# Optimization experiments

Hardware: AMD Instinct MI355X
Metric: run time of the kernel (lower is better)

## Reference

```python
import math
import jax, jax.numpy as jnp
import numpy as np

# ---- SLAYER neuron / simulation constants (from config) ----
THETA = 10.0      # spike threshold
TAU_SR = 10.0     # PSP (SRM) kernel time constant
TAU_REF = 1.0     # refractory kernel time constant
TS = 1.0          # simulation time step
T_SAMPLE = 500    # number of time bins
B, N_IN, N_HID, N_OUT = 64, 1024, 1024, 10


def _alpha_kernel(tau, mult, eps=0.01):
    """slayer _calculateAlphaKernel: mult * t/tau * exp(1 - t/tau), truncated."""
    vals = []
    t = 0.0
    while t < T_SAMPLE:
        v = mult * t / tau * math.exp(1.0 - t / tau)
        if abs(v) < eps and t > tau:
            break
        vals.append(v)
        t += TS
    return np.asarray(vals, np.float32)

SRM_KERNEL = jnp.asarray(_alpha_kernel(TAU_SR, 1.0))            # [K]
REF_KERNEL = jnp.asarray(_alpha_kernel(TAU_REF, -2.0 * THETA))  # [Kr], REF_KERNEL[0] == 0


def dense(x, W):
    # per-timestep fully-connected layer (slayer.dense == 1x1x1 conv3d, no bias)
    # x: [B, Nin, T], W: [Nout, Nin] -> [B, Nout, T]
    return jnp.einsum('oi,bit->bot', W, x)


def psp(x):
    # causal temporal convolution with the SRM kernel: out[t] = Ts * sum_k srm[k] * x[t-k]
    Bx, N, T = x.shape
    K = SRM_KERNEL.shape[0]
    k = SRM_KERNEL[::-1].reshape(1, 1, K).astype(x.dtype)  # flip -> true convolution
    y = jax.lax.conv_general_dilated(
        x.reshape(Bx * N, 1, T), k, (1,), [(K - 1, 0)],
        dimension_numbers=('NCH', 'OIH', 'NCH'))
    return y.reshape(Bx, N, T) * TS


def spike_impl(u_in):
    # sequential LIF thresholding with refractory feedback (slayer spike kernel)
    # u_in: [B, N, T] membrane drive; returns (spikes, membrane) both [B, N, T]
    Kr = REF_KERNEL.shape[0]
    # buf[j] is the refractory contribution arriving at step t+j; new spike at t
    # contributes REF_KERNEL[j] at t+j (REF_KERNEL[0]==0), i.e. shifted kernel into buf.
    refk = jnp.concatenate([REF_KERNEL[1:], jnp.zeros((1,), u_in.dtype)]).astype(u_in.dtype)
    buf0 = jnp.zeros(u_in.shape[:-1] + (Kr,), u_in.dtype)

    def step(buf, u_t):
        u = u_t + buf[..., 0]                              # membrane at time t
        s = (u >= THETA).astype(u_in.dtype) / TS           # spike (amplitude 1/Ts)
        buf = jnp.concatenate([buf[..., 1:], jnp.zeros_like(buf[..., :1])], axis=-1)
        buf = buf + s[..., None] * refk
        return buf, (s, u)

    _, (s, u) = jax.lax.scan(step, buf0, jnp.moveaxis(u_in, -1, 0))
    return jnp.moveaxis(s, 0, -1), jnp.moveaxis(u, 0, -1)


def setup_inputs() -> dict:
    key = jax.random.key(0)
    k1, k2, k3 = jax.random.split(key, 3)
    spike_input = (jax.random.uniform(k1, (B, N_IN, T_SAMPLE)) < 0.05).astype(jnp.float32)
    W1 = jax.random.normal(k2, (N_HID, N_IN), jnp.float32) * 0.3
    W2 = jax.random.normal(k3, (N_OUT, N_HID), jnp.float32) * 0.3
    return {"spike_input": spike_input, "W1": W1, "W2": W2}


def reference(spike_input, W1, W2):
    s1, _ = spike_impl(psp(dense(spike_input, W1)))
    s2, _ = spike_impl(psp(dense(s1, W2)))
    return s2
```

## Files before the change

kernel.cpp:

```cpp
#include <hip/hip_runtime.h>
#include <stdint.h>
#include <math.h>

#define T_SIM 500
#define NB    64
#define NIN   1024
#define NHID  1024
#define NOUT  10
#define KSRM  77
#define CHUNK 32
#define TT5   12
#define NT5   42
#define RINGN 104

__device__ __forceinline__ double srm_tap(int k) {
  double u = (double)k / 10.0;
  double v = u * exp(1.0 - u);
  return (double)(float)v;
}
__device__ __forceinline__ double ref_tap(int j) {
  double v = (-20.0 * (double)j) * exp(1.0 - (double)j);
  return (double)(float)v;
}

__global__ __launch_bounds__(64)
void k_pack(const float* __restrict__ x, unsigned long long* __restrict__ bits) {
  const int b = blockIdx.x, ig = blockIdx.y, tc = blockIdx.z;
  const int lane = threadIdx.x;
  const float* xr = x + ((size_t)b * NIN + ig * 64 + lane) * T_SIM;
  const int t0 = tc * 100;
  for (int t = t0; t < t0 + 100; t += 4) {
    const float4 v = *(const float4*)(xr + t);
    unsigned long long m0 = __ballot(v.x > 0.5f);
    unsigned long long m1 = __ballot(v.y > 0.5f);
    unsigned long long m2 = __ballot(v.z > 0.5f);
    unsigned long long m3 = __ballot(v.w > 0.5f);
    if (lane == 0) {
      unsigned long long* w = bits + (size_t)(b * T_SIM + t) * 16 + ig;
      w[0] = m0; w[16] = m1; w[32] = m2; w[48] = m3;
    }
  }
}

__global__ __launch_bounds__(256)
void k_transpose(const float* __restrict__ W1, float* __restrict__ W1T) {
  __shared__ float tile[64][65];
  const int bo = blockIdx.x * 64, bi = blockIdx.y * 64;
  for (int k = threadIdx.x; k < 4096; k += 256) {
    int r = k >> 6, c = k & 63;
    tile[r][c] = W1[(size_t)(bo + r) * NIN + bi + c];
  }
  __syncthreads();
  for (int k = threadIdx.x; k < 4096; k += 256) {
    int r = k >> 6, c = k & 63;
    W1T[(size_t)(bi + r) * NHID + bo + c] = tile[c][r];
  }
}

__global__ __launch_bounds__(128)
void k_dense1(const uint32_t* __restrict__ bits, const float* __restrict__ W1T,
              double* __restrict__ a1c, int col_base) {
  __shared__ int list[NIN];
  __shared__ int nact_s;
  const int col_loc = blockIdx.x;
  const int tid = threadIdx.x;
  if (tid < 32) {
    uint32_t w = bits[(size_t)(col_base + col_loc) * 32 + tid];
    int c = __popc(w);
    int p = c;
#pragma unroll
    for (int d = 1; d < 32; d <<= 1) {
      int q = __shfl_up(p, d);
      if (tid >= d) p += q;
    }
    int excl = p - c;
    while (w) {
      const int j = __ffs(w) - 1;
      w &= w - 1;
      list[excl++] = tid * 32 + j;
    }
    if (tid == 31) nact_s = excl;
  }
  __syncthreads();
  const int n = nact_s;
  const int o = blockIdx.y * 512 + tid * 4;
  double ax[4] = {0,0,0,0}, ay[4] = {0,0,0,0};
  double az[4] = {0,0,0,0}, aw[4] = {0,0,0,0};
  float4 L[8];
  int g = 0;
  if (n >= 8) {
#pragma unroll
    for (int r = 0; r < 8; ++r)
      L[r] = *(const float4*)(W1T + (size_t)list[r] * NHID + o);
    for (g = 0; g + 16 <= n; g += 8) {
      float4 Nb[8];
#pragma unroll
      for (int r = 0; r < 8; ++r)
        Nb[r] = *(const float4*)(W1T + (size_t)list[g + 8 + r] * NHID + o);
#pragma unroll
      for (int r = 0; r < 8; ++r) {
        const int s = r & 3;
        ax[s] += (double)L[r].x; ay[s] += (double)L[r].y;
        az[s] += (double)L[r].z; aw[s] += (double)L[r].w;
      }
#pragma unroll
      for (int r = 0; r < 8; ++r) L[r] = Nb[r];
    }
#pragma unroll
    for (int r = 0; r < 8; ++r) {
      const int s = r & 3;
      ax[s] += (double)L[r].x; ay[s] += (double)L[r].y;
      az[s] += (double)L[r].z; aw[s] += (double)L[r].w;
    }
    g += 8;
  }
  for (; g < n; ++g) {
    const float4 wv = *(const float4*)(W1T + (size_t)list[g] * NHID + o);
    const int s = g & 3;
    ax[s] += (double)wv.x; ay[s] += (double)wv.y;
    az[s] += (double)wv.z; aw[s] += (double)wv.w;
  }
  double* dst = a1c + (size_t)col_loc * NHID + o;
  __builtin_nontemporal_store((ax[0] + ax[1]) + (ax[2] + ax[3]), dst + 0);
  __builtin_nontemporal_store((ay[0] + ay[1]) + (ay[2] + ay[3]), dst + 1);
  __builtin_nontemporal_store((az[0] + az[1]) + (az[2] + az[3]), dst + 2);
  __builtin_nontemporal_store((aw[0] + aw[1]) + (aw[2] + aw[3]), dst + 3);
}

__global__ __launch_bounds__(448)
void k_ps1(const double* __restrict__ a1c, uint32_t* __restrict__ s1w,
           int b_base) {
  __shared__ double S[RINGN * 32];
  __shared__ double Yp[2][4][TT5 * 32];
  __shared__ double TB[80];
  const int ng = blockIdx.x, b_loc = blockIdx.y;
  const int tid = threadIdx.x;
  const double* __restrict__ abase = a1c + (size_t)b_loc * T_SIM * NHID + ng * 32;
  uint32_t* __restrict__ sbase = s1w + (size_t)(b_base + b_loc) * T_SIM * 32 + ng;

  if (tid < 80) TB[tid] = (tid <= 76) ? srm_tap(tid) : 0.0;
  for (int i = tid; i < RINGN * 32; i += 448) S[i] = 0.0;
  __syncthreads();
  for (int id = tid; id < TT5 * 32; id += 448) {
    const int r = id >> 5, nn = id & 31;
    S[r * 32 + nn] = abase[(size_t)r * NHID + nn];
  }

  const bool isFIR = (tid < 384);
  const int g   = tid / 96;
  const int rem = tid - g * 96;
  const int q   = rem >> 5;
  const int n   = rem & 31;
  double tap[20];
  __syncthreads();
  if (isFIR) {
#pragma unroll
    for (int j = 0; j < 20; ++j) tap[j] = TB[20 * g + j];
  }
  double refk[11];
#pragma unroll
  for (int j = 1; j <= 10; ++j) refk[j] = ref_tap(j);
  uint32_t smask = 0;

  for (int k = 0; k < NT5; ++k) {
    const int t0 = k * TT5;
    const int tv = (T_SIM - t0 < TT5) ? (T_SIM - t0) : TT5;
    const int t0n = t0 + TT5;
    const int tvn = (t0n >= T_SIM) ? 0 : ((T_SIM - t0n < TT5) ? (T_SIM - t0n) : TT5);
    if (isFIR) {
      double pf = 0.0;
      const int pr = tid >> 5, pn = tid & 31;
      const bool hasPf = (tid < tvn * 32);
      if (hasPf) pf = abase[(size_t)(t0n + pr) * NHID + pn];
      const int tb = t0 + q * 4;
      int slot = (tb - 20 * g - 19 + 10400) % RINGN;
      double a0 = 0, a1 = 0, a2 = 0, a3 = 0;
#pragma unroll
      for (int s = 0; s < 23; ++s) {
        const double v = S[slot * 32 + n];
        slot = slot + 1;
        if (slot == RINGN) slot = 0;
        if (s <= 19)           a0 += tap[19 - s] * v;
        if (s >= 1 && s <= 20) a1 += tap[20 - s] * v;
        if (s >= 2 && s <= 21) a2 += tap[21 - s] * v;
        if (s >= 3)            a3 += tap[22 - s] * v;
      }
      double* Yk = Yp[k & 1][g];
      const int tl = q * 4;
      if (tl + 0 < tv) Yk[(tl + 0) * 32 + n] = a0;
      if (tl + 1 < tv) Yk[(tl + 1) * 32 + n] = a1;
      if (tl + 2 < tv) Yk[(tl + 2) * 32 + n] = a2;
      if (tl + 3 < tv) Yk[(tl + 3) * 32 + n] = a3;
      if (hasPf) S[((t0n + pr) % RINGN) * 32 + pn] = pf;
    } else if (k > 0) {
      const int lane = tid - 384;
      if (lane < 32) {
        const int t0p = t0 - TT5;
        const double* Y0 = Yp[(k - 1) & 1][0];
        const double* Y1 = Yp[(k - 1) & 1][1];
        const double* Y2 = Yp[(k - 1) & 1][2];
        const double* Y3 = Yp[(k - 1) & 1][3];
        for (int gg = 0; gg < TT5; ++gg) {
          double u = (Y0[gg * 32 + lane] + Y1[gg * 32 + lane]) +
                     (Y2[gg * 32 + lane] + Y3[gg * 32 + lane]);
#pragma unroll
          for (int j = 10; j >= 1; --j)
            u += refk[j] * (double)((smask >> (j - 1)) & 1u);
          const bool sp = (u >= 10.0);
          smask = (smask << 1) | (sp ? 1u : 0u);
          const unsigned long long bm = __ballot(sp);
          if (lane == 0) sbase[(size_t)(t0p + gg) * 32] = (uint32_t)bm;
        }
      }
    }
    __syncthreads();
  }
  if (!isFIR) {
    const int lane = tid - 384;
    if (lane < 32) {
      const int t0p = (NT5 - 1) * TT5;
      const int tvp = T_SIM - t0p;
      const double* Y0 = Yp[(NT5 - 1) & 1][0];
      const double* Y1 = Yp[(NT5 - 1) & 1][1];
      const double* Y2 = Yp[(NT5 - 1) & 1][2];
      const double* Y3 = Yp[(NT5 - 1) & 1][3];
      for (int gg = 0; gg < tvp; ++gg) {
        double u = (Y0[gg * 32 + lane] + Y1[gg * 32 + lane]) +
                   (Y2[gg * 32 + lane] + Y3[gg * 32 + lane]);
#pragma unroll
        for (int j = 10; j >= 1; --j)
          u += refk[j] * (double)((smask >> (j - 1)) & 1u);
        const bool sp = (u >= 10.0);
        smask = (smask << 1) | (sp ? 1u : 0u);
        const unsigned long long bm = __ballot(sp);
        if (lane == 0) sbase[(size_t)(t0p + gg) * 32] = (uint32_t)bm;
      }
    }
  }
}

__global__ __launch_bounds__(256)
void k_dense2(const uint32_t* __restrict__ s1w,
              const float* __restrict__ W2, double* __restrict__ a2) {
  __shared__ float w2t[NHID * NOUT];
  for (int k = threadIdx.x; k < NHID * NOUT; k += 256) {
    const int o = k >> 10, i = k & 1023;
    w2t[i * NOUT + o] = W2[k];
  }
  __syncthreads();
  const int col = blockIdx.x * 256 + threadIdx.x;
  double acc[NOUT];
#pragma unroll
  for (int o = 0; o < NOUT; ++o) acc[o] = 0.0;
  const uint32_t* w = s1w + (size_t)col * 32;
  for (int wi = 0; wi < 32; ++wi) {
    uint32_t m = w[wi];
    const int ibase = wi * 32;
    while (m) {
      const int j = __ffs(m) - 1;
      m &= m - 1;
      const float* row = &w2t[(ibase + j) * NOUT];
#pragma unroll
      for (int o = 0; o < NOUT; ++o) acc[o] += (double)row[o];
    }
  }
  double* outp = a2 + (size_t)col * NOUT;
#pragma unroll
  for (int o = 0; o < NOUT; ++o) outp[o] = acc[o];
}

__global__ __launch_bounds__(256)
void k_l2(const double* __restrict__ a2, float* __restrict__ out) {
  __shared__ double S[T_SIM * NOUT];
  __shared__ double Y[T_SIM * NOUT];
  __shared__ double srm[KSRM];
  const int b = blockIdx.x, tid = threadIdx.x;
  if (tid < KSRM) srm[tid] = srm_tap(tid);
  for (int i = tid; i < T_SIM * NOUT; i += 256)
    S[i] = a2[(size_t)b * T_SIM * NOUT + i];
  __syncthreads();
  for (int i = tid; i < T_SIM * NOUT; i += 256) {
    const int t = i / 10, o = i - t * 10;
    const int kmax = (t < KSRM - 1) ? t : (KSRM - 1);
    double acc = 0.0;
    for (int k = 0; k <= kmax; ++k)
      acc += srm[k] * S[(t - k) * 10 + o];
    Y[i] = acc;
  }
  __syncthreads();
  if (tid < NOUT) {
    double refk[11];
#pragma unroll
    for (int j = 1; j <= 10; ++j) refk[j] = ref_tap(j);
    uint32_t smask = 0;
    float* op = out + ((size_t)b * NOUT + tid) * T_SIM;
    for (int t = 0; t < T_SIM; ++t) {
      double u = Y[t * 10 + tid];
#pragma unroll
      for (int j = 10; j >= 1; --j)
        u += refk[j] * (double)((smask >> (j - 1)) & 1u);
      const bool sp = (u >= 10.0);
      smask = (smask << 1) | (sp ? 1u : 0u);
      op[t] = sp ? 1.0f : 0.0f;
    }
  }
}

extern "C" void kernel_launch(void* const* d_in, const int* in_sizes, int n_in,
                              void* d_out, int out_size, void* d_ws, size_t ws_size,
                              hipStream_t stream) {
  const float* x  = (const float*)d_in[0];
  const float* W1 = (const float*)d_in[1];
  const float* W2 = (const float*)d_in[2];
  float* out = (float*)d_out;

  char* ws = (char*)d_ws;
  unsigned long long* bits1 = (unsigned long long*)(ws);
  float*  W1T = (float*) (ws + 4096000);
  double* a1c = (double*)(ws + 8290304);
  uint32_t* s1w = (uint32_t*)(ws + 139362304);
  double* a2  = (double*)(ws + 143458304);

  hipLaunchKernelGGL(k_pack, dim3(NB, 16, 5), dim3(64), 0, stream, x, bits1);
  hipLaunchKernelGGL(k_transpose, dim3(16, 16), dim3(256), 0, stream, W1, W1T);

  for (int bc = 0; bc < NB; bc += CHUNK) {
    hipLaunchKernelGGL(k_dense1, dim3(CHUNK * T_SIM, 2), dim3(128), 0, stream,
                       (const uint32_t*)bits1, W1T, a1c, bc * T_SIM);
    hipLaunchKernelGGL(k_ps1, dim3(32, CHUNK), dim3(448), 0, stream,
                       a1c, s1w, bc);
  }

  hipLaunchKernelGGL(k_dense2, dim3(125), dim3(256), 0, stream, s1w, W2, a2);
  hipLaunchKernelGGL(k_l2, dim3(NB), dim3(256), 0, stream, a2, out);
}
```

Before: 956.9 us.

## Fuse dense1 and PSP/spike stages into one kernel pipelined across double-buffered chunks

Merges the dense1 and PSP/spike kernels into a single kernel whose blocks are split by block index into dense-column work and PSP work. Chunk c's dense accumulation runs concurrently with chunk c-1's PSP/spike pass, using two ping-pong activation buffers. The batch chunk is halved to 16 and the dense part now uses 256 of the 448 threads with one block per column, so the PSP stage's serial latency is meant to hide under dense throughput. In exchange, 192 threads sit idle in every dense block, and the shared-memory union and 448-thread launch bounds may lower occupancy.

```diff
diff --git a/kernel.cpp b/kernel.cpp
--- a/kernel.cpp
+++ b/kernel.cpp
@@ -8,10 +8,11 @@
 #define NHID  1024
 #define NOUT  10
 #define KSRM  77
-#define CHUNK 32
+#define CHUNK 16
 #define TT5   12
 #define NT5   42
 #define RINGN 104
+#define NGW   32
 
 __device__ __forceinline__ double srm_tap(int k) {
   double u = (double)k / 10.0;
@@ -57,152 +58,122 @@
   }
 }
 
-__global__ __launch_bounds__(128)
-void k_dense1(const uint32_t* __restrict__ bits, const float* __restrict__ W1T,
-              double* __restrict__ a1c, int col_base) {
-  __shared__ int list[NIN];
-  __shared__ int nact_s;
-  const int col_loc = blockIdx.x;
+__global__ __launch_bounds__(448, 4)
+void k_fused(const uint32_t* __restrict__ bits, const float* __restrict__ W1T,
+             double* __restrict__ aw, const double* __restrict__ ar,
+             uint32_t* __restrict__ s1w, int col_base, int ndense, int nps1,
+             int b_base) {
+  __shared__ union U {
+    struct { double S[RINGN * NGW]; double Yp[2][4][TT5 * NGW]; double TB[80]; } p;
+    struct { int list[NIN]; int nact; } d;
+  } sh;
+  const int bid = blockIdx.x;
   const int tid = threadIdx.x;
-  if (tid < 32) {
-    uint32_t w = bits[(size_t)(col_base + col_loc) * 32 + tid];
-    int c = __popc(w);
-    int p = c;
-#pragma unroll
-    for (int d = 1; d < 32; d <<= 1) {
-      int q = __shfl_up(p, d);
-      if (tid >= d) p += q;
-    }
-    int excl = p - c;
-    while (w) {
-      const int j = __ffs(w) - 1;
-      w &= w - 1;
-      list[excl++] = tid * 32 + j;
-    }
-    if (tid == 31) nact_s = excl;
-  }
-  __syncthreads();
-  const int n = nact_s;
-  const int o = blockIdx.y * 512 + tid * 4;
-  double ax[4] = {0,0,0,0}, ay[4] = {0,0,0,0};
-  double az[4] = {0,0,0,0}, aw[4] = {0,0,0,0};
-  float4 L[8];
-  int g = 0;
-  if (n >= 8) {
-#pragma unroll
-    for (int r = 0; r < 8; ++r)
-      L[r] = *(const float4*)(W1T + (size_t)list[r] * NHID + o);
-    for (g = 0; g + 16 <= n; g += 8) {
-      float4 Nb[8];
-#pragma unroll
-      for (int r = 0; r < 8; ++r)
-        Nb[r] = *(const float4*)(W1T + (size_t)list[g + 8 + r] * NHID + o);
-#pragma unroll
-      for (int r = 0; r < 8; ++r) {
-        const int s = r & 3;
-        ax[s] += (double)L[r].x; ay[s] += (double)L[r].y;
-        az[s] += (double)L[r].z; aw[s] += (double)L[r].w;
+  int dcol = -1, pblk = -1;
+  if (ndense && nps1) {
+    const int q = bid / 17, r = bid - 17 * q;
+    if (r == 16) pblk = q; else dcol = q * 16 + r;
+  } else if (nps1) {
+    pblk = bid;
+  } else {
+    dcol = bid;
+  }
+
+  if (pblk >= 0) {
+    if (pblk >= nps1) return;
+    const int ng = pblk & 31, b_loc = pblk >> 5;
+    const double* __restrict__ abase = ar + (size_t)b_loc * T_SIM * NHID + ng * NGW;
+    uint32_t* __restrict__ sbase = s1w + (size_t)(b_base + b_loc) * T_SIM * 32 + ng;
+
+    if (tid < 80) sh.p.TB[tid] = (tid <= 76) ? srm_tap(tid) : 0.0;
+    for (int i = tid; i < RINGN * NGW; i += 448) sh.p.S[i] = 0.0;
+    __syncthreads();
+    for (int id = tid; id < TT5 * NGW; id += 448) {
+      const int r = id >> 5, nn = id & 31;
+      sh.p.S[r * NGW + nn] = abase[(size_t)r * NHID + nn];
+    }
+
+    const bool isFIR = (tid < 384);
+    const int g   = tid / 96;
+    const int rem = tid - g * 96;
+    const int q   = rem >> 5;
+    const int n   = rem & 31;
+    double tap[20];
+    __syncthreads();
+    if (isFIR) {
+#pragma unroll
+      for (int j = 0; j < 20; ++j) tap[j] = sh.p.TB[20 * g + j];
+    }
+    double refk[11];
+#pragma unroll
+    for (int j = 1; j <= 10; ++j) refk[j] = ref_tap(j);
+    uint32_t smask = 0;
+
+    for (int k = 0; k < NT5; ++k) {
+      const int t0 = k * TT5;
+      const int tv = (T_SIM - t0 < TT5) ? (T_SIM - t0) : TT5;
+      const int t0n = t0 + TT5;
+      const int tvn = (t0n >= T_SIM) ? 0 : ((T_SIM - t0n < TT5) ? (T_SIM - t0n) : TT5);
+      if (isFIR) {
+        double pf = 0.0;
+        const int pr = tid >> 5, pn = tid & 31;
+        const bool hasPf = (tid < tvn * NGW);
+        if (hasPf) pf = abase[(size_t)(t0n + pr) * NHID + pn];
+        const int tb = t0 + q * 4;
+        int slot = (tb - 20 * g - 19 + 10400) % RINGN;
+        double a0 = 0, a1 = 0, a2 = 0, a3 = 0;
+#pragma unroll
+        for (int s = 0; s < 23; ++s) {
+          const double v = sh.p.S[slot * NGW + n];
+          slot = slot + 1;
+          if (slot == RINGN) slot = 0;
+          if (s <= 19)           a0 += tap[19 - s] * v;
+          if (s >= 1 && s <= 20) a1 += tap[20 - s] * v;
+          if (s >= 2 && s <= 21) a2 += tap[21 - s] * v;
+          if (s >= 3)            a3 += tap[22 - s] * v;
+        }
+        double* Yk = sh.p.Yp[k & 1][g];
+        const int tl = q * 4;
+        if (tl + 0 < tv) Yk[(tl + 0) * NGW + n] = a0;
+        if (tl + 1 < tv) Yk[(tl + 1) * NGW + n] = a1;
+        if (tl + 2 < tv) Yk[(tl + 2) * NGW + n] = a2;
+        if (tl + 3 < tv) Yk[(tl + 3) * NGW + n] = a3;
+        if (hasPf) sh.p.S[((t0n + pr) % RINGN) * NGW + pn] = pf;
+      } else if (k > 0) {
+        const int lane = tid - 384;
+        if (lane < 32) {
+          const int t0p = t0 - TT5;
+          const double* Y0 = sh.p.Yp[(k - 1) & 1][0];
+          const double* Y1 = sh.p.Yp[(k - 1) & 1][1];
+          const double* Y2 = sh.p.Yp[(k - 1) & 1][2];
+          const double* Y3 = sh.p.Yp[(k - 1) & 1][3];
+          for (int gg = 0; gg < TT5; ++gg) {
+            double u = (Y0[gg * NGW + lane] + Y1[gg * NGW + lane]) +
+                       (Y2[gg * NGW + lane] + Y3[gg * NGW + lane]);
+#pragma unroll
+            for (int j = 10; j >= 1; --j)
+              u += refk[j] * (double)((smask >> (j - 1)) & 1u);
+            const bool sp = (u >= 10.0);
+            smask = (smask << 1) | (sp ? 1u : 0u);
+            const unsigned long long bm = __ballot(sp);
+            if (lane == 0) sbase[(size_t)(t0p + gg) * 32] = (uint32_t)bm;
+          }
+        }
       }
-#pragma unroll
-      for (int r = 0; r < 8; ++r) L[r] = Nb[r];
-    }
-#pragma unroll
-    for (int r = 0; r < 8; ++r) {
-      const int s = r & 3;
-      ax[s] += (double)L[r].x; ay[s] += (double)L[r].y;
-      az[s] += (double)L[r].z; aw[s] += (double)L[r].w;
-    }
-    g += 8;
-  }
-  for (; g < n; ++g) {
-    const float4 wv = *(const float4*)(W1T + (size_t)list[g] * NHID + o);
-    const int s = g & 3;
-    ax[s] += (double)wv.x; ay[s] += (double)wv.y;
-    az[s] += (double)wv.z; aw[s] += (double)wv.w;
-  }
-  double* dst = a1c + (size_t)col_loc * NHID + o;
-  __builtin_nontemporal_store((ax[0] + ax[1]) + (ax[2] + ax[3]), dst + 0);
-  __builtin_nontemporal_store((ay[0] + ay[1]) + (ay[2] + ay[3]), dst + 1);
-  __builtin_nontemporal_store((az[0] + az[1]) + (az[2] + az[3]), dst + 2);
-  __builtin_nontemporal_store((aw[0] + aw[1]) + (aw[2] + aw[3]), dst + 3);
-}
-
-__global__ __launch_bounds__(448)
-void k_ps1(const double* __restrict__ a1c, uint32_t* __restrict__ s1w,
-           int b_base) {
-  __shared__ double S[RINGN * 32];
-  __shared__ double Yp[2][4][TT5 * 32];
-  __shared__ double TB[80];
-  const int ng = blockIdx.x, b_loc = blockIdx.y;
-  const int tid = threadIdx.x;
-  const double* __restrict__ abase = a1c + (size_t)b_loc * T_SIM * NHID + ng * 32;
-  uint32_t* __restrict__ sbase = s1w + (size_t)(b_base + b_loc) * T_SIM * 32 + ng;
-
-  if (tid < 80) TB[tid] = (tid <= 76) ? srm_tap(tid) : 0.0;
-  for (int i = tid; i < RINGN * 32; i += 448) S[i] = 0.0;
-  __syncthreads();
-  for (int id = tid; id < TT5 * 32; id += 448) {
-    const int r = id >> 5, nn = id & 31;
-    S[r * 32 + nn] = abase[(size_t)r * NHID + nn];
-  }
-
-  const bool isFIR = (tid < 384);
-  const int g   = tid / 96;
-  const int rem = tid - g * 96;
-  const int q   = rem >> 5;
-  const int n   = rem & 31;
-  double tap[20];
-  __syncthreads();
-  if (isFIR) {
-#pragma unroll
-    for (int j = 0; j < 20; ++j) tap[j] = TB[20 * g + j];
-  }
-  double refk[11];
-#pragma unroll
-  for (int j = 1; j <= 10; ++j) refk[j] = ref_tap(j);
-  uint32_t smask = 0;
-
-  for (int k = 0; k < NT5; ++k) {
-    const int t0 = k * TT5;
-    const int tv = (T_SIM - t0 < TT5) ? (T_SIM - t0) : TT5;
-    const int t0n = t0 + TT5;
-    const int tvn = (t0n >= T_SIM) ? 0 : ((T_SIM - t0n < TT5) ? (T_SIM - t0n) : TT5);
-    if (isFIR) {
-      double pf = 0.0;
-      const int pr = tid >> 5, pn = tid & 31;
-      const bool hasPf = (tid < tvn * 32);
-      if (hasPf) pf = abase[(size_t)(t0n + pr) * NHID + pn];
-      const int tb = t0 + q * 4;
-      int slot = (tb - 20 * g - 19 + 10400) % RINGN;
-      double a0 = 0, a1 = 0, a2 = 0, a3 = 0;
-#pragma unroll
-      for (int s = 0; s < 23; ++s) {
-        const double v = S[slot * 32 + n];
-        slot = slot + 1;
-        if (slot == RINGN) slot = 0;
-        if (s <= 19)           a0 += tap[19 - s] * v;
-        if (s >= 1 && s <= 20) a1 += tap[20 - s] * v;
-        if (s >= 2 && s <= 21) a2 += tap[21 - s] * v;
-        if (s >= 3)            a3 += tap[22 - s] * v;
-      }
-      double* Yk = Yp[k & 1][g];
-      const int tl = q * 4;
-      if (tl + 0 < tv) Yk[(tl + 0) * 32 + n] = a0;
-      if (tl + 1 < tv) Yk[(tl + 1) * 32 + n] = a1;
-      if (tl + 2 < tv) Yk[(tl + 2) * 32 + n] = a2;
-      if (tl + 3 < tv) Yk[(tl + 3) * 32 + n] = a3;
-      if (hasPf) S[((t0n + pr) % RINGN) * 32 + pn] = pf;
-    } else if (k > 0) {
+      __syncthreads();
+    }
+    if (!isFIR) {
       const int lane = tid - 384;
       if (lane < 32) {
-        const int t0p = t0 - TT5;
-        const double* Y0 = Yp[(k - 1) & 1][0];
-        const double* Y1 = Yp[(k - 1) & 1][1];
-        const double* Y2 = Yp[(k - 1) & 1][2];
-        const double* Y3 = Yp[(k - 1) & 1][3];
-        for (int gg = 0; gg < TT5; ++gg) {
-          double u = (Y0[gg * 32 + lane] + Y1[gg * 32 + lane]) +
-                     (Y2[gg * 32 + lane] + Y3[gg * 32 + lane]);
+        const int t0p = (NT5 - 1) * TT5;
+        const int tvp = T_SIM - t0p;
+        const double* Y0 = sh.p.Yp[(NT5 - 1) & 1][0];
+        const double* Y1 = sh.p.Yp[(NT5 - 1) & 1][1];
+        const double* Y2 = sh.p.Yp[(NT5 - 1) & 1][2];
+        const double* Y3 = sh.p.Yp[(NT5 - 1) & 1][3];
+        for (int gg = 0; gg < tvp; ++gg) {
+          double u = (Y0[gg * NGW + lane] + Y1[gg * NGW + lane]) +
+                     (Y2[gg * NGW + lane] + Y3[gg * NGW + lane]);
 #pragma unroll
           for (int j = 10; j >= 1; --j)
             u += refk[j] * (double)((smask >> (j - 1)) & 1u);
@@ -213,29 +184,73 @@
         }
       }
     }
-    __syncthreads();
-  }
-  if (!isFIR) {
-    const int lane = tid - 384;
-    if (lane < 32) {
-      const int t0p = (NT5 - 1) * TT5;
-      const int tvp = T_SIM - t0p;
-      const double* Y0 = Yp[(NT5 - 1) & 1][0];
-      const double* Y1 = Yp[(NT5 - 1) & 1][1];
-      const double* Y2 = Yp[(NT5 - 1) & 1][2];
-      const double* Y3 = Yp[(NT5 - 1) & 1][3];
-      for (int gg = 0; gg < tvp; ++gg) {
-        double u = (Y0[gg * 32 + lane] + Y1[gg * 32 + lane]) +
-                   (Y2[gg * 32 + lane] + Y3[gg * 32 + lane]);
-#pragma unroll
-        for (int j = 10; j >= 1; --j)
-          u += refk[j] * (double)((smask >> (j - 1)) & 1u);
-        const bool sp = (u >= 10.0);
-        smask = (smask << 1) | (sp ? 1u : 0u);
-        const unsigned long long bm = __ballot(sp);
-        if (lane == 0) sbase[(size_t)(t0p + gg) * 32] = (uint32_t)bm;
+    return;
+  }
+
+  if (dcol >= ndense) return;
+  const int col_loc = dcol;
+  if (tid < 32) {
+    uint32_t w = bits[(size_t)(col_base + col_loc) * 32 + tid];
+    int c = __popc(w);
+    int p = c;
+#pragma unroll
+    for (int d = 1; d < 32; d <<= 1) {
+      int qq = __shfl_up(p, d);
+      if (tid >= d) p += qq;
+    }
+    int excl = p - c;
+    while (w) {
+      const int j = __ffs(w) - 1;
+      w &= w - 1;
+      sh.d.list[excl++] = tid * 32 + j;
+    }
+    if (tid == 31) sh.d.nact = excl;
+  }
+  __syncthreads();
+  if (tid < 256) {
+    const int n = sh.d.nact;
+    const int o = tid * 4;
+    double ax[4] = {0,0,0,0}, ay[4] = {0,0,0,0};
+    double az[4] = {0,0,0,0}, aw4[4] = {0,0,0,0};
+    float4 L[8];
+    int g = 0;
+    if (n >= 8) {
+#pragma unroll
+      for (int r = 0; r < 8; ++r)
+        L[r] = *(const float4*)(W1T + (size_t)sh.d.list[r] * NHID + o);
+      for (g = 0; g + 16 <= n; g += 8) {
+        float4 Nb[8];
+#pragma unroll
+        for (int r = 0; r < 8; ++r)
+          Nb[r] = *(const float4*)(W1T + (size_t)sh.d.list[g + 8 + r] * NHID + o);
+#pragma unroll
+        for (int r = 0; r < 8; ++r) {
+          const int s = r & 3;
+          ax[s] += (double)L[r].x; ay[s] += (double)L[r].y;
+          az[s] += (double)L[r].z; aw4[s] += (double)L[r].w;
+        }
+#pragma unroll
+        for (int r = 0; r < 8; ++r) L[r] = Nb[r];
       }
-    }
+#pragma unroll
+      for (int r = 0; r < 8; ++r) {
+        const int s = r & 3;
+        ax[s] += (double)L[r].x; ay[s] += (double)L[r].y;
+        az[s] += (double)L[r].z; aw4[s] += (double)L[r].w;
+      }
+      g += 8;
+    }
+    for (; g < n; ++g) {
+      const float4 wv = *(const float4*)(W1T + (size_t)sh.d.list[g] * NHID + o);
+      const int s = g & 3;
+      ax[s] += (double)wv.x; ay[s] += (double)wv.y;
+      az[s] += (double)wv.z; aw4[s] += (double)wv.w;
+    }
+    double* dst = aw + (size_t)col_loc * NHID + o;
+    __builtin_nontemporal_store((ax[0] + ax[1]) + (ax[2] + ax[3]), dst + 0);
+    __builtin_nontemporal_store((ay[0] + ay[1]) + (ay[2] + ay[3]), dst + 1);
+    __builtin_nontemporal_store((az[0] + az[1]) + (az[2] + az[3]), dst + 2);
+    __builtin_nontemporal_store((aw4[0] + aw4[1]) + (aw4[2] + aw4[3]), dst + 3);
   }
 }
 
@@ -316,20 +331,29 @@
 
   char* ws = (char*)d_ws;
   unsigned long long* bits1 = (unsigned long long*)(ws);
-  float*  W1T = (float*) (ws + 4096000);
-  double* a1c = (double*)(ws + 8290304);
+  float*  W1T = (float*)(ws + 4096000);
+  double* abuf0 = (double*)(ws + 8290304);
+  double* abuf1 = (double*)(ws + 73826304);
   uint32_t* s1w = (uint32_t*)(ws + 139362304);
   double* a2  = (double*)(ws + 143458304);
+  double* abuf[2] = {abuf0, abuf1};
 
   hipLaunchKernelGGL(k_pack, dim3(NB, 16, 5), dim3(64), 0, stream, x, bits1);
   hipLaunchKernelGGL(k_transpose, dim3(16, 16), dim3(256), 0, stream, W1, W1T);
 
-  for (int bc = 0; bc < NB; bc += CHUNK) {
-    hipLaunchKernelGGL(k_dense1, dim3(CHUNK * T_SIM, 2), dim3(128), 0, stream,
-                       (const uint32_t*)bits1, W1T, a1c, bc * T_SIM);
-    hipLaunchKernelGGL(k_ps1, dim3(32, CHUNK), dim3(448), 0, stream,
-                       a1c, s1w, bc);
-  }
+  const int NDB = CHUNK * T_SIM;
+  const int NPB = 32 * CHUNK;
+  hipLaunchKernelGGL(k_fused, dim3(NDB), dim3(448), 0, stream,
+                     (const uint32_t*)bits1, W1T, abuf[0], abuf[1], s1w,
+                     0, NDB, 0, 0);
+  for (int c = 1; c < 4; ++c) {
+    hipLaunchKernelGGL(k_fused, dim3(17 * NPB), dim3(448), 0, stream,
+                       (const uint32_t*)bits1, W1T, abuf[c & 1], abuf[(c ^ 1) & 1],
+                       s1w, c * NDB, NDB, NPB, (c - 1) * CHUNK);
+  }
+  hipLaunchKernelGGL(k_fused, dim3(NPB), dim3(448), 0, stream,
+                     (const uint32_t*)bits1, W1T, abuf[0], abuf[1], s1w,
+                     0, 0, NPB, 3 * CHUNK);
 
   hipLaunchKernelGGL(k_dense2, dim3(125), dim3(256), 0, stream, s1w, W2, a2);
   hipLaunchKernelGGL(k_l2, dim3(NB), dim3(256), 0, stream, a2, out);
```

After: 1.285 ms. 34.3% more time.
